# Kernel optimization log

Measured on AMD Instinct MI355X. Metric: run time of the kernel, lower is better.

Reference implementation:

```python
import jax, jax.numpy as jnp
import numpy as np

LEVELS = 256

def setup_inputs() -> dict:
    key = jax.random.key(0)
    # pixel values in [0, 256), already uint8-range ints (original casts to uint8)
    x = jax.random.randint(key, (64, 786432), 0, LEVELS, dtype=jnp.int32)
    return {"x": x}

def reference(x):
    # Per-sample 256-bin histogram over all pixels (cv2.calcHist equivalent),
    # implemented as an atomic-add scatter per row via vmap.
    B = x.shape[0]

    def hist_one(row):  # row: [N] int32 in [0, LEVELS)
        return jnp.zeros((LEVELS,), dtype=jnp.float32).at[row].add(1.0)

    hist = jax.vmap(hist_one)(x)  # [B, LEVELS]
    # cv2.calcHist returns shape (LEVELS, 1); assignment into a (LEVELS, LEVELS)
    # slot broadcasts the histogram column across all 256 columns.
    out = jnp.broadcast_to(hist[:, :, None], (B, LEVELS, LEVELS))
    # original returns a list containing this single stacked tensor
    return out
```

## Files before the change

kernel.cpp:

```cpp
#include <hip/hip_runtime.h>

#define LEVELS 256
#define NROWS 64
#define ROWLEN 786432
#define CHUNKS 32
#define CHUNK_ELEMS (ROWLEN / CHUNKS)
#define BLOCK 256
#define WAVES (BLOCK / 64)

__global__ __launch_bounds__(256) void zero_ws_kernel(unsigned int* __restrict__ ws) {
    int i = blockIdx.x * blockDim.x + threadIdx.x;
    if (i < NROWS * LEVELS) ws[i] = 0u;
}

__global__ __launch_bounds__(256) void hist_kernel(const int* __restrict__ x,
                                                   unsigned int* __restrict__ ws) {
    __shared__ unsigned int lhist[WAVES][LEVELS];

    const int row   = blockIdx.y;
    const int chunk = blockIdx.x;
    const int tid   = threadIdx.x;
    const int wave  = tid >> 6;

    unsigned int* flat = &lhist[0][0];
    for (int i = tid; i < WAVES * LEVELS; i += BLOCK) flat[i] = 0u;
    __syncthreads();

    const int4* xr = (const int4*)(x + (long)row * ROWLEN + (long)chunk * CHUNK_ELEMS);
    const int n4 = CHUNK_ELEMS / 4;
    unsigned int* h = lhist[wave];
    for (int i = tid; i < n4; i += 2 * BLOCK) {
        int4 a = xr[i];
        int4 b = xr[i + BLOCK];
        atomicAdd(&h[a.x & 255], 1u);
        atomicAdd(&h[a.y & 255], 1u);
        atomicAdd(&h[a.z & 255], 1u);
        atomicAdd(&h[a.w & 255], 1u);
        atomicAdd(&h[b.x & 255], 1u);
        atomicAdd(&h[b.y & 255], 1u);
        atomicAdd(&h[b.z & 255], 1u);
        atomicAdd(&h[b.w & 255], 1u);
    }
    __syncthreads();

    for (int bin = tid; bin < LEVELS; bin += BLOCK) {
        unsigned int s = 0u;
        #pragma unroll
        for (int w = 0; w < WAVES; ++w) s += lhist[w][bin];
        if (s) atomicAdd(&ws[row * LEVELS + bin], s);
    }
}

__global__ __launch_bounds__(256) void broadcast_kernel(const unsigned int* __restrict__ ws,
                                                        float* __restrict__ out) {
    long i  = (long)blockIdx.x * BLOCK + threadIdx.x;
    long bv = i >> 6;
    float val = (float)ws[bv];
    ((float4*)out)[i] = make_float4(val, val, val, val);
}

extern "C" void kernel_launch(void* const* d_in, const int* in_sizes, int n_in,
                              void* d_out, int out_size, void* d_ws, size_t ws_size,
                              hipStream_t stream) {
    const int* x = (const int*)d_in[0];
    float* out = (float*)d_out;
    unsigned int* ws = (unsigned int*)d_ws;

    zero_ws_kernel<<<(NROWS * LEVELS + BLOCK - 1) / BLOCK, BLOCK, 0, stream>>>(ws);

    dim3 grid(CHUNKS, NROWS);
    hist_kernel<<<grid, BLOCK, 0, stream>>>(x, ws);

    long total4 = (long)NROWS * LEVELS * LEVELS / 4;
    broadcast_kernel<<<(int)(total4 / BLOCK), BLOCK, 0, stream>>>(ws, out);
}
```

Before: 279.2 us.

## Write per-chunk partial histograms and fuse the reduction into the broadcast kernel

Each histogram block now stores its 256-bin partial result to its own slot in the workspace instead of atomically adding into a shared per-row histogram. The separate zeroing kernel is dropped. A new kernel sums the 32 chunk partials for each bin with wave shuffles, then writes the broadcast float row. This removes one launch and the global atomics. In exchange the workspace grows, and the broadcast kernel gains a strided gather over partials.

```diff
diff --git a/kernel.cpp b/kernel.cpp
--- a/kernel.cpp
+++ b/kernel.cpp
@@ -8,13 +8,8 @@
 #define BLOCK 256
 #define WAVES (BLOCK / 64)
 
-__global__ __launch_bounds__(256) void zero_ws_kernel(unsigned int* __restrict__ ws) {
-    int i = blockIdx.x * blockDim.x + threadIdx.x;
-    if (i < NROWS * LEVELS) ws[i] = 0u;
-}
-
-__global__ __launch_bounds__(256) void hist_kernel(const int* __restrict__ x,
-                                                   unsigned int* __restrict__ ws) {
+__global__ __launch_bounds__(256) void hist_partial_kernel(const int* __restrict__ x,
+                                                           unsigned int* __restrict__ ws) {
     __shared__ unsigned int lhist[WAVES][LEVELS];
 
     const int row   = blockIdx.y;
@@ -43,20 +38,30 @@
     }
     __syncthreads();
 
+    unsigned int* dst = ws + ((long)(row * CHUNKS + chunk)) * LEVELS;
     for (int bin = tid; bin < LEVELS; bin += BLOCK) {
         unsigned int s = 0u;
         #pragma unroll
         for (int w = 0; w < WAVES; ++w) s += lhist[w][bin];
-        if (s) atomicAdd(&ws[row * LEVELS + bin], s);
+        dst[bin] = s;
     }
 }
 
-__global__ __launch_bounds__(256) void broadcast_kernel(const unsigned int* __restrict__ ws,
-                                                        float* __restrict__ out) {
-    long i  = (long)blockIdx.x * BLOCK + threadIdx.x;
-    long bv = i >> 6;
-    float val = (float)ws[bv];
-    ((float4*)out)[i] = make_float4(val, val, val, val);
+__global__ __launch_bounds__(256) void reduce_broadcast_kernel(const unsigned int* __restrict__ ws,
+                                                               float* __restrict__ out) {
+    const int b    = blockIdx.x >> 6;
+    const int vg   = blockIdx.x & 63;
+    const int wave = threadIdx.x >> 6;
+    const int lane = threadIdx.x & 63;
+    const int bin  = vg * 4 + wave;
+
+    unsigned int v = ws[((long)(b * CHUNKS) + (lane & 31)) * LEVELS + bin];
+    #pragma unroll
+    for (int m = 1; m <= 16; m <<= 1) v += (unsigned int)__shfl_xor((int)v, m);
+    float val = (float)v;
+
+    float4* dst = (float4*)(out + ((long)b * LEVELS + bin) * LEVELS);
+    dst[lane] = make_float4(val, val, val, val);
 }
 
 extern "C" void kernel_launch(void* const* d_in, const int* in_sizes, int n_in,
@@ -66,11 +71,8 @@
     float* out = (float*)d_out;
     unsigned int* ws = (unsigned int*)d_ws;
 
-    zero_ws_kernel<<<(NROWS * LEVELS + BLOCK - 1) / BLOCK, BLOCK, 0, stream>>>(ws);
+    dim3 grid(CHUNKS, NROWS);
+    hist_partial_kernel<<<grid, BLOCK, 0, stream>>>(x, ws);
 
-    dim3 grid(CHUNKS, NROWS);
-    hist_kernel<<<grid, BLOCK, 0, stream>>>(x, ws);
-
-    long total4 = (long)NROWS * LEVELS * LEVELS / 4;
-    broadcast_kernel<<<(int)(total4 / BLOCK), BLOCK, 0, stream>>>(ws, out);
+    reduce_broadcast_kernel<<<NROWS * 64, BLOCK, 0, stream>>>(ws, out);
 }
```

Result: no change. 278.6 us (-0.2%).
